# Kernel optimization log

Measured on AMD Instinct MI355X. Metric: run time of the kernel, lower is better.

## Reference

```python
import math
import jax, jax.numpy as jnp
import numpy as np

THETA = 2.0 ** 16
TWO_PI = 2.0 * math.pi


def _freqs(N):
    # quantize(arange(N), 2) = floor(t/2)*2 -> paired frequencies
    idx = jnp.floor(jnp.arange(N, dtype=jnp.float32) / 2.0) * 2.0
    return 1.0 / (THETA ** (idx / N)) / TWO_PI  # (N,)


def _rope(v, cos, sin):
    # rotate pairs: (-v_odd, v_even) interleaved back to original layout
    v_rot = jnp.stack((-v[..., 1::2], v[..., ::2]), axis=-1).reshape(v.shape)
    return v * cos + v_rot * sin


def setup_inputs() -> dict:
    key = jax.random.key(0)
    k1, k2 = jax.random.split(key)
    B, nh, T, N, D = 1, 4, 2048, 8192, 256
    Q = jax.random.normal(k1, (B, nh, T, N), dtype=jnp.float32) * 0.02
    V = jax.random.normal(k2, (B, 1, T, D), dtype=jnp.float32)
    return {"Q": Q, "V": V}


def reference(Q, V):
    # Q: (B, nh, T, N) sparse neuron space; V: (B, 1, T, D) embedding space; K is Q
    T, N = Q.shape[2], Q.shape[3]
    freqs = _freqs(N)
    phases = jnp.arange(T, dtype=jnp.float32)[:, None] * freqs[None, :]  # (T, N)
    ang = (phases % 1.0) * TWO_PI
    cos, sin = jnp.cos(ang), jnp.sin(ang)
    QR = _rope(Q, cos, sin)  # (B, nh, T, N)
    scores = jnp.einsum('bhtn,bhsn->bhts', QR, QR)  # (B, nh, T, T)
    causal = jnp.tril(jnp.ones((T, T), dtype=bool), k=-1)  # strictly lower
    scores = jnp.where(causal, scores, 0.0)
    # V broadcasts over heads: (B, nh, T, T) @ (B, 1, T, D) -> (B, nh, T, D)
    return jnp.matmul(scores, V)
```

## Files before the change

kernel.cpp:

```cpp
#include <hip/hip_runtime.h>

#define LDS_AS __attribute__((address_space(3)))
#define GLB_AS __attribute__((address_space(1)))

typedef __attribute__((ext_vector_type(8))) short bf16x8;
typedef __attribute__((ext_vector_type(4))) float f32x4;

static constexpr int NH = 4;
static constexpr int T  = 2048;
static constexpr int N  = 8192;
static constexpr int D  = 256;

__device__ inline unsigned short f2bf(float f) {
    unsigned int u = __float_as_uint(f);
    u += 0x7FFFu + ((u >> 16) & 1u);
    return (unsigned short)(u >> 16);
}

__device__ inline void gl2lds16(const void* g, void* l) {
    __builtin_amdgcn_global_load_lds((GLB_AS void*)g, (LDS_AS void*)l, 16, 0, 0);
}

__global__ void rope_kernel(const float* __restrict__ Q, unsigned short* __restrict__ QR) {
    int g = blockIdx.x * 256 + threadIdx.x;
    int base = g << 2;
    int n = base & (N - 1);
    int t = (base >> 13) & (T - 1);
    const float4 q = *(const float4*)(Q + (size_t)base);
    float tf = (float)t;
    const float inv2pi = 0.15915494309189535f;
    float f0 = exp2f((float)n       * (-1.0f / 512.0f)) * inv2pi;
    float f1 = exp2f((float)(n + 2) * (-1.0f / 512.0f)) * inv2pi;
    float r0 = tf * f0; r0 -= floorf(r0);
    float r1 = tf * f1; r1 -= floorf(r1);
    float s0 = __builtin_amdgcn_sinf(r0), c0 = __builtin_amdgcn_cosf(r0);
    float s1 = __builtin_amdgcn_sinf(r1), c1 = __builtin_amdgcn_cosf(r1);
    ushort4 o;
    o.x = f2bf(q.x * c0 - q.y * s0);
    o.y = f2bf(q.y * c0 + q.x * s0);
    o.z = f2bf(q.z * c1 - q.w * s1);
    o.w = f2bf(q.w * c1 + q.z * s1);
    *(ushort4*)(QR + (size_t)base) = o;
}

__global__ void vt_kernel(const float* __restrict__ V, unsigned short* __restrict__ Vt) {
    __shared__ unsigned short tile[64 * 65];
    int tb = blockIdx.x >> 2, db = blockIdx.x & 3;
    int t0 = tb * 64, d0 = db * 64;
    int tid = threadIdx.x;
    #pragma unroll
    for (int r = 0; r < 16; r++) {
        int idx = tid + r * 256;
        int tl = idx >> 6, dl = idx & 63;
        tile[tl * 65 + dl] = f2bf(V[(size_t)(t0 + tl) * D + d0 + dl]);
    }
    __syncthreads();
    #pragma unroll
    for (int r = 0; r < 16; r++) {
        int idx = tid + r * 256;
        int dl = idx >> 6, tl = idx & 63;
        Vt[(size_t)(d0 + dl) * T + t0 + tl] = tile[tl * 65 + dl];
    }
}

__global__ __launch_bounds__(256) void gemm1_kernel(const unsigned short* __restrict__ QR,
                                                    unsigned short* __restrict__ S, int KS) {
    __shared__ __align__(16) unsigned short As[128 * 32];
    __shared__ __align__(16) unsigned short Bs[128 * 32];

    int bx = blockIdx.x;
    int per_h = 136 * KS;
    int h = bx / per_h;
    int rem = bx % per_h;
    int pair = rem / KS;
    int ks = rem % KS;
    int bi = 0;
    while (((bi + 1) * (bi + 2)) / 2 <= pair) bi++;
    int bj = pair - (bi * (bi + 1)) / 2;

    const unsigned short* A = QR + (size_t)h * T * N + (size_t)bi * 128 * N;
    const unsigned short* B = QR + (size_t)h * T * N + (size_t)bj * 128 * N;

    int KN = N / KS;
    int k_begin = ks * KN, k_end = k_begin + KN;

    int tid = threadIdx.x;
    int lane = tid & 63, wave = tid >> 6;
    int wm = wave >> 1, wn = wave & 1;
    int quad = lane >> 4, l16 = lane & 15;
    int srow = tid >> 2;
    int scol = (tid & 3) * 8;

    f32x4 acc[4][4];
    #pragma unroll
    for (int i = 0; i < 4; i++)
        #pragma unroll
        for (int j = 0; j < 4; j++)
            #pragma unroll
            for (int r = 0; r < 4; r++) acc[i][j][r] = 0.0f;

    for (int k0 = k_begin; k0 < k_end; k0 += 32) {
        __syncthreads();
        gl2lds16(A + (size_t)srow * N + k0 + scol,        &As[srow * 32 + scol]);
        gl2lds16(A + (size_t)(srow + 64) * N + k0 + scol, &As[(srow + 64) * 32 + scol]);
        gl2lds16(B + (size_t)srow * N + k0 + scol,        &Bs[srow * 32 + scol]);
        gl2lds16(B + (size_t)(srow + 64) * N + k0 + scol, &Bs[(srow + 64) * 32 + scol]);
        __syncthreads();

        bf16x8 a[4], b[4];
        #pragma unroll
        for (int i = 0; i < 4; i++) {
            a[i] = *(const bf16x8*)&As[(wm * 64 + i * 16 + l16) * 32 + quad * 8];
            b[i] = *(const bf16x8*)&Bs[(wn * 64 + i * 16 + l16) * 32 + quad * 8];
        }
        #pragma unroll
        for (int i = 0; i < 4; i++)
            #pragma unroll
            for (int j = 0; j < 4; j++)
                acc[i][j] = __builtin_amdgcn_mfma_f32_16x16x32_bf16(a[i], b[j], acc[i][j], 0, 0, 0);
    }

    unsigned short* Sh = S + (size_t)ks * NH * T * T + (size_t)h * T * T;
    #pragma unroll
    for (int i = 0; i < 4; i++) {
        int t_base = bi * 128 + wm * 64 + i * 16 + quad * 4;
        #pragma unroll
        for (int j = 0; j < 4; j++) {
            int s_g = bj * 128 + wn * 64 + j * 16 + l16;
            #pragma unroll
            for (int r = 0; r < 4; r++) {
                int t_g = t_base + r;
                float v = (s_g < t_g) ? acc[i][j][r] : 0.0f;
                Sh[(size_t)t_g * T + s_g] = f2bf(v);
            }
        }
    }
}

__global__ __launch_bounds__(256) void gemm2_kernel(const unsigned short* __restrict__ S,
                                                    const unsigned short* __restrict__ Vt,
                                                    float* __restrict__ out, int KS) {
    __shared__ __align__(16) unsigned short As[128 * 32];
    __shared__ __align__(16) unsigned short Bs[128 * 32];

    int bx = blockIdx.x;
    int per_h = 2 * KS * 40;
    int h = bx / per_h;
    int rem = bx % per_h;
    int dblk = rem / (KS * 40);
    int rem2 = rem % (KS * 40);
    int ks = rem2 / 40;
    int tc = rem2 % 40;
    int bi = 0, cum = 0;
    for (; bi < 16; bi++) { int nc = (bi + 4) >> 2; if (cum + nc > tc) break; cum += nc; }
    int c = tc - cum;

    int kend = (bi + 1) * 128;
    int cstart = c * 512;
    int clen = min(512, kend - cstart);

    const unsigned short* A = S + (size_t)ks * NH * T * T + (size_t)h * T * T
                                + (size_t)bi * 128 * T + cstart;
    const unsigned short* B = Vt + (size_t)dblk * 128 * T + cstart;

    int tid = threadIdx.x;
    int lane = tid & 63, wave = tid >> 6;
    int wm = wave >> 1, wn = wave & 1;
    int quad = lane >> 4, l16 = lane & 15;
    int srow = tid >> 2;
    int scol = (tid & 3) * 8;

    f32x4 acc[4][4];
    #pragma unroll
    for (int i = 0; i < 4; i++)
        #pragma unroll
        for (int j = 0; j < 4; j++)
            #pragma unroll
            for (int r = 0; r < 4; r++) acc[i][j][r] = 0.0f;

    for (int k0 = 0; k0 < clen; k0 += 32) {
        __syncthreads();
        gl2lds16(A + (size_t)srow * T + k0 + scol,        &As[srow * 32 + scol]);
        gl2lds16(A + (size_t)(srow + 64) * T + k0 + scol, &As[(srow + 64) * 32 + scol]);
        gl2lds16(B + (size_t)srow * T + k0 + scol,        &Bs[srow * 32 + scol]);
        gl2lds16(B + (size_t)(srow + 64) * T + k0 + scol, &Bs[(srow + 64) * 32 + scol]);
        __syncthreads();

        bf16x8 a[4], b[4];
        #pragma unroll
        for (int i = 0; i < 4; i++) {
            a[i] = *(const bf16x8*)&As[(wm * 64 + i * 16 + l16) * 32 + quad * 8];
            b[i] = *(const bf16x8*)&Bs[(wn * 64 + i * 16 + l16) * 32 + quad * 8];
        }
        #pragma unroll
        for (int i = 0; i < 4; i++)
            #pragma unroll
            for (int j = 0; j < 4; j++)
                acc[i][j] = __builtin_amdgcn_mfma_f32_16x16x32_bf16(a[i], b[j], acc[i][j], 0, 0, 0);
    }

    float* oh = out + (size_t)h * T * D;
    #pragma unroll
    for (int i = 0; i < 4; i++) {
        int t_base = bi * 128 + wm * 64 + i * 16 + quad * 4;
        #pragma unroll
        for (int j = 0; j < 4; j++) {
            int d_g = dblk * 128 + wn * 64 + j * 16 + l16;
            #pragma unroll
            for (int r = 0; r < 4; r++) {
                int t_g = t_base + r;
                atomicAdd(&oh[(size_t)t_g * D + d_g], acc[i][j][r]);
            }
        }
    }
}

extern "C" void kernel_launch(void* const* d_in, const int* in_sizes, int n_in,
                              void* d_out, int out_size, void* d_ws, size_t ws_size,
                              hipStream_t stream) {
    const float* Q = (const float*)d_in[0];
    const float* V = (const float*)d_in[1];
    float* out = (float*)d_out;

    const size_t qr_elems = (size_t)NH * T * N;
    const size_t vt_elems = (size_t)D * T;
    const size_t s_elems  = (size_t)NH * T * T;

    int KS = (ws_size >= (qr_elems + vt_elems + 2 * s_elems) * sizeof(unsigned short)) ? 2 : 1;
    if (ws_size < (qr_elems + vt_elems + (size_t)KS * s_elems) * sizeof(unsigned short)) return;

    unsigned short* QR = (unsigned short*)d_ws;
    unsigned short* Vt = QR + qr_elems;
    unsigned short* S  = Vt + vt_elems;

    rope_kernel<<<(NH * T * N / 4) / 256, 256, 0, stream>>>(Q, QR);
    vt_kernel<<<(T / 64) * (D / 64), 256, 0, stream>>>(V, Vt);
    gemm1_kernel<<<NH * 136 * KS, 256, 0, stream>>>(QR, S, KS);
    hipMemsetAsync(d_out, 0, (size_t)out_size * sizeof(float), stream);
    gemm2_kernel<<<NH * 2 * KS * 40, 256, 0, stream>>>(S, Vt, out, KS);
}
```

Before: 622.5 us.

## Widen gemm1 tiles to 128x256 with double-buffered LDS and fold split-K in gemm2

gemm1 now computes 128x256 output tiles, with 72 triangular tasks per head instead of 136. It double-buffers the LDS loads so the next k-slice is prefetched while MFMAs run on the current one, and it streams B fragments to cut register pressure. Split-K can now go up to 4 when workspace allows. gemm2 sums the split-K partials inside each block instead of launching separate blocks per split. The goals are more operand reuse, overlap of load latency with compute, and fewer atomics in gemm2, at the cost of more LDS and accumulator registers and more wasted work on diagonal tiles.

```diff
diff --git a/kernel.cpp b/kernel.cpp
--- a/kernel.cpp
+++ b/kernel.cpp
@@ -63,26 +63,27 @@
     }
 }
 
-__global__ __launch_bounds__(256) void gemm1_kernel(const unsigned short* __restrict__ QR,
-                                                    unsigned short* __restrict__ S, int KS) {
-    __shared__ __align__(16) unsigned short As[128 * 32];
-    __shared__ __align__(16) unsigned short Bs[128 * 32];
+__global__ __launch_bounds__(256, 2) void gemm1_kernel(const unsigned short* __restrict__ QR,
+                                                       unsigned short* __restrict__ S, int KS) {
+    __shared__ __align__(16) unsigned short As[2][128 * 32];
+    __shared__ __align__(16) unsigned short Bs[2][256 * 32];
 
     int bx = blockIdx.x;
-    int per_h = 136 * KS;
+    int per_h = 72 * KS;
     int h = bx / per_h;
     int rem = bx % per_h;
-    int pair = rem / KS;
+    int task = rem / KS;
     int ks = rem % KS;
-    int bi = 0;
-    while (((bi + 1) * (bi + 2)) / 2 <= pair) bi++;
-    int bj = pair - (bi * (bi + 1)) / 2;
+    int bi = 0, cum = 0;
+    for (; bi < 16; bi++) { int nb = (bi >> 1) + 1; if (cum + nb > task) break; cum += nb; }
+    int bj = task - cum;
 
     const unsigned short* A = QR + (size_t)h * T * N + (size_t)bi * 128 * N;
-    const unsigned short* B = QR + (size_t)h * T * N + (size_t)bj * 128 * N;
+    const unsigned short* B = QR + (size_t)h * T * N + (size_t)bj * 256 * N;
 
     int KN = N / KS;
-    int k_begin = ks * KN, k_end = k_begin + KN;
+    int k_begin = ks * KN;
+    int nit = KN / 32;
 
     int tid = threadIdx.x;
     int lane = tid & 63, wave = tid >> 6;
@@ -91,33 +92,48 @@
     int srow = tid >> 2;
     int scol = (tid & 3) * 8;
 
-    f32x4 acc[4][4];
+    f32x4 acc[4][8];
     #pragma unroll
     for (int i = 0; i < 4; i++)
         #pragma unroll
-        for (int j = 0; j < 4; j++)
+        for (int j = 0; j < 8; j++)
             #pragma unroll
             for (int r = 0; r < 4; r++) acc[i][j][r] = 0.0f;
 
-    for (int k0 = k_begin; k0 < k_end; k0 += 32) {
+    {
+        int k0 = k_begin;
+        gl2lds16(A + (size_t)srow * N + k0 + scol,         &As[0][srow * 32 + scol]);
+        gl2lds16(A + (size_t)(srow + 64) * N + k0 + scol,  &As[0][(srow + 64) * 32 + scol]);
+        gl2lds16(B + (size_t)srow * N + k0 + scol,         &Bs[0][srow * 32 + scol]);
+        gl2lds16(B + (size_t)(srow + 64) * N + k0 + scol,  &Bs[0][(srow + 64) * 32 + scol]);
+        gl2lds16(B + (size_t)(srow + 128) * N + k0 + scol, &Bs[0][(srow + 128) * 32 + scol]);
+        gl2lds16(B + (size_t)(srow + 192) * N + k0 + scol, &Bs[0][(srow + 192) * 32 + scol]);
+    }
+
+    for (int it = 0; it < nit; it++) {
+        int cur = it & 1, nxt = cur ^ 1;
         __syncthreads();
-        gl2lds16(A + (size_t)srow * N + k0 + scol,        &As[srow * 32 + scol]);
-        gl2lds16(A + (size_t)(srow + 64) * N + k0 + scol, &As[(srow + 64) * 32 + scol]);
-        gl2lds16(B + (size_t)srow * N + k0 + scol,        &Bs[srow * 32 + scol]);
-        gl2lds16(B + (size_t)(srow + 64) * N + k0 + scol, &Bs[(srow + 64) * 32 + scol]);
-        __syncthreads();
-
-        bf16x8 a[4], b[4];
-        #pragma unroll
-        for (int i = 0; i < 4; i++) {
-            a[i] = *(const bf16x8*)&As[(wm * 64 + i * 16 + l16) * 32 + quad * 8];
-            b[i] = *(const bf16x8*)&Bs[(wn * 64 + i * 16 + l16) * 32 + quad * 8];
-        }
+        if (it + 1 < nit) {
+            int k0 = k_begin + (it + 1) * 32;
+            gl2lds16(A + (size_t)srow * N + k0 + scol,         &As[nxt][srow * 32 + scol]);
+            gl2lds16(A + (size_t)(srow + 64) * N + k0 + scol,  &As[nxt][(srow + 64) * 32 + scol]);
+            gl2lds16(B + (size_t)srow * N + k0 + scol,         &Bs[nxt][srow * 32 + scol]);
+            gl2lds16(B + (size_t)(srow + 64) * N + k0 + scol,  &Bs[nxt][(srow + 64) * 32 + scol]);
+            gl2lds16(B + (size_t)(srow + 128) * N + k0 + scol, &Bs[nxt][(srow + 128) * 32 + scol]);
+            gl2lds16(B + (size_t)(srow + 192) * N + k0 + scol, &Bs[nxt][(srow + 192) * 32 + scol]);
+        }
+
+        bf16x8 a[4];
         #pragma unroll
         for (int i = 0; i < 4; i++)
-            #pragma unroll
-            for (int j = 0; j < 4; j++)
-                acc[i][j] = __builtin_amdgcn_mfma_f32_16x16x32_bf16(a[i], b[j], acc[i][j], 0, 0, 0);
+            a[i] = *(const bf16x8*)&As[cur][(wm * 64 + i * 16 + l16) * 32 + quad * 8];
+        #pragma unroll
+        for (int j = 0; j < 8; j++) {
+            bf16x8 b = *(const bf16x8*)&Bs[cur][(wn * 128 + j * 16 + l16) * 32 + quad * 8];
+            #pragma unroll
+            for (int i = 0; i < 4; i++)
+                acc[i][j] = __builtin_amdgcn_mfma_f32_16x16x32_bf16(a[i], b, acc[i][j], 0, 0, 0);
+        }
     }
 
     unsigned short* Sh = S + (size_t)ks * NH * T * T + (size_t)h * T * T;
@@ -125,8 +141,8 @@
     for (int i = 0; i < 4; i++) {
         int t_base = bi * 128 + wm * 64 + i * 16 + quad * 4;
         #pragma unroll
-        for (int j = 0; j < 4; j++) {
-            int s_g = bj * 128 + wn * 64 + j * 16 + l16;
+        for (int j = 0; j < 8; j++) {
+            int s_g = bj * 256 + wn * 128 + j * 16 + l16;
             #pragma unroll
             for (int r = 0; r < 4; r++) {
                 int t_g = t_base + r;
@@ -144,13 +160,11 @@
     __shared__ __align__(16) unsigned short Bs[128 * 32];
 
     int bx = blockIdx.x;
-    int per_h = 2 * KS * 40;
+    int per_h = 2 * 40;
     int h = bx / per_h;
     int rem = bx % per_h;
-    int dblk = rem / (KS * 40);
-    int rem2 = rem % (KS * 40);
-    int ks = rem2 / 40;
-    int tc = rem2 % 40;
+    int dblk = rem / 40;
+    int tc = rem % 40;
     int bi = 0, cum = 0;
     for (; bi < 16; bi++) { int nc = (bi + 4) >> 2; if (cum + nc > tc) break; cum += nc; }
     int c = tc - cum;
@@ -159,8 +173,6 @@
     int cstart = c * 512;
     int clen = min(512, kend - cstart);
 
-    const unsigned short* A = S + (size_t)ks * NH * T * T + (size_t)h * T * T
-                                + (size_t)bi * 128 * T + cstart;
     const unsigned short* B = Vt + (size_t)dblk * 128 * T + cstart;
 
     int tid = threadIdx.x;
@@ -178,25 +190,29 @@
             #pragma unroll
             for (int r = 0; r < 4; r++) acc[i][j][r] = 0.0f;
 
-    for (int k0 = 0; k0 < clen; k0 += 32) {
-        __syncthreads();
-        gl2lds16(A + (size_t)srow * T + k0 + scol,        &As[srow * 32 + scol]);
-        gl2lds16(A + (size_t)(srow + 64) * T + k0 + scol, &As[(srow + 64) * 32 + scol]);
-        gl2lds16(B + (size_t)srow * T + k0 + scol,        &Bs[srow * 32 + scol]);
-        gl2lds16(B + (size_t)(srow + 64) * T + k0 + scol, &Bs[(srow + 64) * 32 + scol]);
-        __syncthreads();
-
-        bf16x8 a[4], b[4];
-        #pragma unroll
-        for (int i = 0; i < 4; i++) {
-            a[i] = *(const bf16x8*)&As[(wm * 64 + i * 16 + l16) * 32 + quad * 8];
-            b[i] = *(const bf16x8*)&Bs[(wn * 64 + i * 16 + l16) * 32 + quad * 8];
-        }
-        #pragma unroll
-        for (int i = 0; i < 4; i++)
-            #pragma unroll
-            for (int j = 0; j < 4; j++)
-                acc[i][j] = __builtin_amdgcn_mfma_f32_16x16x32_bf16(a[i], b[j], acc[i][j], 0, 0, 0);
+    for (int ks = 0; ks < KS; ks++) {
+        const unsigned short* A = S + (size_t)ks * NH * T * T + (size_t)h * T * T
+                                    + (size_t)bi * 128 * T + cstart;
+        for (int k0 = 0; k0 < clen; k0 += 32) {
+            __syncthreads();
+            gl2lds16(A + (size_t)srow * T + k0 + scol,        &As[srow * 32 + scol]);
+            gl2lds16(A + (size_t)(srow + 64) * T + k0 + scol, &As[(srow + 64) * 32 + scol]);
+            gl2lds16(B + (size_t)srow * T + k0 + scol,        &Bs[srow * 32 + scol]);
+            gl2lds16(B + (size_t)(srow + 64) * T + k0 + scol, &Bs[(srow + 64) * 32 + scol]);
+            __syncthreads();
+
+            bf16x8 a[4], b[4];
+            #pragma unroll
+            for (int i = 0; i < 4; i++) {
+                a[i] = *(const bf16x8*)&As[(wm * 64 + i * 16 + l16) * 32 + quad * 8];
+                b[i] = *(const bf16x8*)&Bs[(wn * 64 + i * 16 + l16) * 32 + quad * 8];
+            }
+            #pragma unroll
+            for (int i = 0; i < 4; i++)
+                #pragma unroll
+                for (int j = 0; j < 4; j++)
+                    acc[i][j] = __builtin_amdgcn_mfma_f32_16x16x32_bf16(a[i], b[j], acc[i][j], 0, 0, 0);
+        }
     }
 
     float* oh = out + (size_t)h * T * D;
@@ -226,7 +242,12 @@
     const size_t vt_elems = (size_t)D * T;
     const size_t s_elems  = (size_t)NH * T * T;
 
-    int KS = (ws_size >= (qr_elems + vt_elems + 2 * s_elems) * sizeof(unsigned short)) ? 2 : 1;
+    int KS = 1;
+    for (int cand : {4, 2, 1}) {
+        if (ws_size >= (qr_elems + vt_elems + (size_t)cand * s_elems) * sizeof(unsigned short)) {
+            KS = cand; break;
+        }
+    }
     if (ws_size < (qr_elems + vt_elems + (size_t)KS * s_elems) * sizeof(unsigned short)) return;
 
     unsigned short* QR = (unsigned short*)d_ws;
@@ -235,7 +256,7 @@
 
     rope_kernel<<<(NH * T * N / 4) / 256, 256, 0, stream>>>(Q, QR);
     vt_kernel<<<(T / 64) * (D / 64), 256, 0, stream>>>(V, Vt);
-    gemm1_kernel<<<NH * 136 * KS, 256, 0, stream>>>(QR, S, KS);
+    gemm1_kernel<<<NH * 72 * KS, 256, 0, stream>>>(QR, S, KS);
     hipMemsetAsync(d_out, 0, (size_t)out_size * sizeof(float), stream);
-    gemm2_kernel<<<NH * 2 * KS * 40, 256, 0, stream>>>(S, Vt, out, KS);
-}
+    gemm2_kernel<<<NH * 2 * 40, 256, 0, stream>>>(S, Vt, out, KS);
+}
```

Result: faster. 605.5 us (-2.7%).
